# Performance work log

Measured on AMD Instinct MI355X. Metric: run time of the kernel, lower is better.

Reference implementation:

```python
import jax, jax.numpy as jnp
import numpy as np

HIDDEN = 1024
NUM_HEAD = 16
HEAD_DIM = HIDDEN // NUM_HEAD


def setup_inputs() -> dict:
    key = jax.random.key(0)
    ks = jax.random.split(key, 9)
    B, S = 1, 4096
    scale = 1.0 / np.sqrt(HIDDEN)
    inp = {
        "x": jax.random.normal(ks[0], (B, S, HIDDEN), dtype=jnp.float32),
        "wq": jax.random.normal(ks[1], (HIDDEN, HIDDEN), dtype=jnp.float32) * scale,
        "bq": jnp.zeros((HIDDEN,), dtype=jnp.float32),
        "wk": jax.random.normal(ks[2], (HIDDEN, HIDDEN), dtype=jnp.float32) * scale,
        "bk": jnp.zeros((HIDDEN,), dtype=jnp.float32),
        "wv": jax.random.normal(ks[3], (HIDDEN, HIDDEN), dtype=jnp.float32) * scale,
        "bv": jnp.zeros((HIDDEN,), dtype=jnp.float32),
        "wo": jax.random.normal(ks[4], (HIDDEN, HIDDEN), dtype=jnp.float32) * scale,
        "bo": jnp.zeros((HIDDEN,), dtype=jnp.float32),
    }
    return inp


def reference(x, wq, bq, wk, bk, wv, bv, wo, bo):
    B, S, _ = x.shape
    # QKV projections (torch Linear: x @ W.T + b)
    def split_heads(t):
        return t.reshape(B, S, NUM_HEAD, HEAD_DIM).transpose(0, 2, 1, 3)  # [B,H,S,D]
    q = split_heads(x @ wq.T + bq)
    k = split_heads(x @ wk.T + bk)
    v = split_heads(x @ wv.T + bv)
    # scaled dot-product scores: [B,H,S,S]
    scores = jnp.einsum('bhsd,bhtd->bhst', q, k) / jnp.sqrt(jnp.float32(HEAD_DIM))
    # faithful double softmax over the key axis (no mask; dropout = eval identity)
    attn = jax.nn.softmax(scores, axis=-1)
    attn = jax.nn.softmax(attn, axis=-1)
    out = jnp.einsum('bhst,bhtd->bhsd', attn, v)  # [B,H,S,D]
    out = out.transpose(0, 2, 1, 3).reshape(B, S, HIDDEN)
    return out @ wo.T + bo
```

## Files before the change

### kernel.cpp

```cpp
#include <hip/hip_runtime.h>
#include <hip/hip_bf16.h>
#include <stdint.h>

#define S 4096
#define HID 1024
#define NH 16
#define DH 64

typedef __attribute__((ext_vector_type(8))) short short8;
typedef __attribute__((ext_vector_type(2))) float f32x2;
typedef __attribute__((ext_vector_type(4))) float f32x4;
typedef __attribute__((ext_vector_type(16))) float f32x16;
typedef __attribute__((ext_vector_type(4))) unsigned int u32x4;

__device__ __forceinline__ unsigned short f2bf(float f) {
  unsigned int u = __builtin_bit_cast(unsigned int, f);
  u += 0x7FFF + ((u >> 16) & 1);
  return (unsigned short)(u >> 16);
}
__device__ __forceinline__ unsigned int pktrunc(float lo, float hi) {
  return __builtin_amdgcn_perm(__builtin_bit_cast(unsigned int, hi),
                               __builtin_bit_cast(unsigned int, lo), 0x07060302u);
}
__device__ __forceinline__ void gload16(const unsigned short* g, unsigned short* l) {
  __builtin_amdgcn_global_load_lds((const __attribute__((address_space(1))) unsigned int*)g,
                                   (__attribute__((address_space(3))) unsigned int*)l, 16, 0, 0);
}

__global__ __launch_bounds__(256) void cast_kernel(
    const float* __restrict__ x,  const float* __restrict__ wq,
    const float* __restrict__ wk, const float* __restrict__ wv,
    const float* __restrict__ wo,
    unsigned short* __restrict__ xb,  unsigned short* __restrict__ wqb,
    unsigned short* __restrict__ wkb, unsigned short* __restrict__ wvb,
    unsigned short* __restrict__ wob)
{
  int y = blockIdx.y;
  const float* src; unsigned short* dst; int n;
  if      (y == 0) { src = x;  dst = xb;  n = S * HID; }
  else if (y == 1) { src = wq; dst = wqb; n = HID * HID; }
  else if (y == 2) { src = wk; dst = wkb; n = HID * HID; }
  else if (y == 3) { src = wv; dst = wvb; n = HID * HID; }
  else             { src = wo; dst = wob; n = HID * HID; }
  int i = (blockIdx.x * 256 + threadIdx.x) * 4;
  if (i < n) {
    float4 v = *reinterpret_cast<const float4*>(src + i);
    ushort4 o;
    o.x = f2bf(v.x); o.y = f2bf(v.y); o.z = f2bf(v.z); o.w = f2bf(v.w);
    *reinterpret_cast<ushort4*>(dst + i) = o;
  }
}

__device__ __forceinline__ void gemm128(
    const unsigned short* __restrict__ A, const unsigned short* __restrict__ W,
    unsigned short* As, unsigned short* Bs, f32x4 acc[4][4], int row0, int col0)
{
  const int tid = threadIdx.x;
  const int wave = tid >> 6, lane = tid & 63, quad = lane >> 4, l16 = lane & 15;
  const int wr = (wave >> 1) * 64, wc = (wave & 1) * 64;
  const int srow = lane >> 2, sseg = lane & 3;
  const f32x4 z = {0.f, 0.f, 0.f, 0.f};
  #pragma unroll
  for (int i = 0; i < 4; i++)
    #pragma unroll
    for (int j = 0; j < 4; j++) acc[i][j] = z;

  for (int k0 = 0; k0 < HID; k0 += 32) {
    __syncthreads();
    #pragma unroll
    for (int c = 0; c < 2; c++) {
      const int rbase = c * 64 + wave * 16;
      gload16(A + (size_t)(row0 + rbase + srow) * HID + k0 + sseg * 8, As + rbase * 32);
      gload16(W + (size_t)(col0 + rbase + srow) * HID + k0 + sseg * 8, Bs + rbase * 32);
    }
    __syncthreads();

    short8 af[4], bfr[4];
    #pragma unroll
    for (int i = 0; i < 4; i++)
      af[i] = *reinterpret_cast<const short8*>(As + (wr + i * 16 + l16) * 32 + quad * 8);
    #pragma unroll
    for (int j = 0; j < 4; j++)
      bfr[j] = *reinterpret_cast<const short8*>(Bs + (wc + j * 16 + l16) * 32 + quad * 8);
    #pragma unroll
    for (int i = 0; i < 4; i++)
      #pragma unroll
      for (int j = 0; j < 4; j++)
        acc[i][j] = __builtin_amdgcn_mfma_f32_16x16x32_bf16(af[i], bfr[j], acc[i][j], 0, 0, 0);
  }
}

__global__ __launch_bounds__(256) void qkv_gemm_kernel(
    const unsigned short* __restrict__ X,
    const unsigned short* __restrict__ Wq, const unsigned short* __restrict__ Wk,
    const unsigned short* __restrict__ Wv,
    const float* __restrict__ bq, const float* __restrict__ bk, const float* __restrict__ bv,
    unsigned short* __restrict__ Qo, unsigned short* __restrict__ K2o, unsigned short* __restrict__ Vbo)
{
  __shared__ unsigned short As[128 * 32];
  __shared__ unsigned short Bs[128 * 32];
  const int zsel = blockIdx.z;
  const unsigned short* W = (zsel == 0) ? Wq : (zsel == 1) ? Wk : Wv;
  const float* bias        = (zsel == 0) ? bq : (zsel == 1) ? bk : bv;
  const int row0 = blockIdx.x * 128, col0 = blockIdx.y * 128;
  f32x4 acc[4][4];
  gemm128(X, W, As, Bs, acc, row0, col0);

  const int tid = threadIdx.x;
  const int wave = tid >> 6, lane = tid & 63, quad = lane >> 4, l16 = lane & 15;
  const int wr = (wave >> 1) * 64, wc = (wave & 1) * 64;

  if (zsel == 0) {
    const float osc = 0.18033688011112042f;
    #pragma unroll
    for (int j = 0; j < 4; j++) {
      int n = col0 + wc + j * 16 + l16;
      float bb = bias[n];
      int h = n >> 6, d = n & 63;
      #pragma unroll
      for (int i = 0; i < 4; i++)
        #pragma unroll
        for (int rr = 0; rr < 4; rr++) {
          int s = row0 + wr + i * 16 + quad * 4 + rr;
          Qo[(size_t)(h * S + s) * DH + d] = f2bf((acc[i][j][rr] + bb) * osc);
        }
    }
  } else if (zsel == 1) {
    #pragma unroll
    for (int j = 0; j < 4; j++) {
      int n = col0 + wc + j * 16 + l16;
      float bb = bias[n];
      int h = n >> 6, dh = n & 63;
      int c = dh >> 4, hfk = (dh >> 3) & 1, j8 = dh & 7;
      #pragma unroll
      for (int i = 0; i < 4; i++)
        #pragma unroll
        for (int rr = 0; rr < 4; rr++) {
          int s = row0 + wr + i * 16 + quad * 4 + rr;
          int g = s >> 5, l32k = s & 31;
          K2o[((size_t)((h * 128 + g) * 4 + c) * 64 + hfk * 32 + l32k) * 8 + j8] =
              f2bf(acc[i][j][rr] + bb);
        }
    }
  } else {
    #pragma unroll
    for (int j = 0; j < 4; j++) {
      int n = col0 + wc + j * 16 + l16;
      float bb = bias[n];
      int h = n >> 6, dh = n & 63;
      int ng = dh >> 5, l32v = dh & 31;
      int hf_v = quad & 1, jj0 = (quad >> 1) * 4;
      #pragma unroll
      for (int i = 0; i < 4; i++) {
        int gt = (row0 + wr + i * 16) >> 5;
        int grp = i & 1;
        ushort4 pv;
        pv.x = f2bf(acc[i][j][0] + bb); pv.y = f2bf(acc[i][j][1] + bb);
        pv.z = f2bf(acc[i][j][2] + bb); pv.w = f2bf(acc[i][j][3] + bb);
        *reinterpret_cast<ushort4*>(
            Vbo + ((size_t)(((h * 128 + gt) * 2 + grp) * 2 + ng) * 64 + hf_v * 32 + l32v) * 8 + jj0) = pv;
      }
    }
  }
}

__global__ __launch_bounds__(256) void out_gemm_kernel(
    const unsigned short* __restrict__ A, const unsigned short* __restrict__ W,
    const float* __restrict__ be, float* __restrict__ dst)
{
  __shared__ unsigned short As[128 * 32];
  __shared__ unsigned short Bs[128 * 32];
  const int row0 = blockIdx.x * 128, col0 = blockIdx.y * 128;
  f32x4 acc[4][4];
  gemm128(A, W, As, Bs, acc, row0, col0);

  const int tid = threadIdx.x;
  const int wave = tid >> 6, lane = tid & 63, quad = lane >> 4, l16 = lane & 15;
  const int wr = (wave >> 1) * 64, wc = (wave & 1) * 64;
  #pragma unroll
  for (int j = 0; j < 4; j++) {
    int n = col0 + wc + j * 16 + l16;
    float bb = be[n];
    #pragma unroll
    for (int i = 0; i < 4; i++)
      #pragma unroll
      for (int rr = 0; rr < 4; rr++) {
        int s = row0 + wr + i * 16 + quad * 4 + rr;
        dst[(size_t)s * HID + n] = acc[i][j][rr] + bb;
      }
  }
}

__global__ __launch_bounds__(256) void vsum_kernel(
    const unsigned short* __restrict__ Vb, float* __restrict__ VsumP)
{
  __shared__ float red[256];
  const int p = blockIdx.x, h = blockIdx.y, tid = threadIdx.x;
  const int d = tid & 63, chunk = tid >> 6;
  const int ng = d >> 5, l32 = d & 31;
  float s = 0.f;
  for (int m = 0; m < 4; m++) {
    int gt = p * 16 + chunk * 4 + m;
    #pragma unroll
    for (int grp = 0; grp < 2; grp++)
      #pragma unroll
      for (int hf = 0; hf < 2; hf++) {
        uint4 u = *reinterpret_cast<const uint4*>(
            Vb + ((size_t)(((h * 128 + gt) * 2 + grp) * 2 + ng) * 64 + hf * 32 + l32) * 8);
        const unsigned int w[4] = {u.x, u.y, u.z, u.w};
        #pragma unroll
        for (int q = 0; q < 4; q++) {
          s += __builtin_bit_cast(float, w[q] << 16);
          s += __builtin_bit_cast(float, w[q] & 0xFFFF0000u);
        }
      }
  }
  red[tid] = s;
  __syncthreads();
  if (tid < 64)
    VsumP[p * 1024 + h * 64 + tid] = red[tid] + red[64 + tid] + red[128 + tid] + red[192 + tid];
}

__global__ __launch_bounds__(256) void biasfold_kernel(
    const float* __restrict__ VsumP, const float* __restrict__ wo,
    const float* __restrict__ bo, float* __restrict__ be)
{
  const int n = blockIdx.x * 4 + (threadIdx.x >> 6);
  const int l = threadIdx.x & 63;
  float acc = 0.f;
  #pragma unroll
  for (int i = 0; i < 16; i++) {
    float vs = 0.f;
    #pragma unroll
    for (int p = 0; p < 8; p++) vs += VsumP[p * 1024 + l + 64 * i];
    acc += vs * wo[(size_t)n * HID + l + 64 * i];
  }
  #pragma unroll
  for (int off = 32; off >= 1; off >>= 1) acc += __shfl_xor(acc, off);
  if (l == 0) be[n] = bo[n] + acc * (1.f / 4097.f);
}

struct AttnState {
  short8 qf[4];
  f32x16 Oa[2];
  f32x16 zacc;
  f32x2  zp;
};

template<int BUF>
__device__ __forceinline__ void attn_compute(
    const unsigned short* kbase, const unsigned short* vbase, AttnState& st)
{
  short8 kf[4], vfr[4];
  #pragma unroll
  for (int c = 0; c < 4; c++)
    kf[c] = *reinterpret_cast<const short8*>(kbase + BUF * 8192 + c * 512);
  #pragma unroll
  for (int w = 0; w < 4; w++)
    vfr[w] = *reinterpret_cast<const short8*>(vbase + BUF * 8192 + w * 512);

  f32x16 acc = __builtin_amdgcn_mfma_f32_32x32x16_bf16(kf[0], st.qf[0], st.zacc, 0, 0, 0);
  #pragma unroll
  for (int c = 1; c < 4; c++)
    acc = __builtin_amdgcn_mfma_f32_32x32x16_bf16(kf[c], st.qf[c], acc, 0, 0, 0);

  unsigned int D[8];
  #pragma unroll
  for (int m = 0; m < 8; m++) {
    float t0 = __builtin_amdgcn_exp2f(acc[2 * m]);
    float t1 = __builtin_amdgcn_exp2f(acc[2 * m + 1]);
    f32x2 t = {t0, t1};
    st.zp += t;
    D[m] = pktrunc(t0, t1);
  }
  u32x4 d0 = {D[0], D[1], D[2], D[3]};
  u32x4 d1 = {D[4], D[5], D[6], D[7]};
  short8 A0 = __builtin_bit_cast(short8, d0);
  short8 A1 = __builtin_bit_cast(short8, d1);

  st.Oa[0] = __builtin_amdgcn_mfma_f32_32x32x16_bf16(A0, vfr[0], st.Oa[0], 0, 0, 0);
  st.Oa[1] = __builtin_amdgcn_mfma_f32_32x32x16_bf16(A0, vfr[1], st.Oa[1], 0, 0, 0);
  st.Oa[0] = __builtin_amdgcn_mfma_f32_32x32x16_bf16(A1, vfr[2], st.Oa[0], 0, 0, 0);
  st.Oa[1] = __builtin_amdgcn_mfma_f32_32x32x16_bf16(A1, vfr[3], st.Oa[1], 0, 0, 0);
}

__device__ __forceinline__ void stage4(const unsigned short* gs, unsigned short* ldst) {
  #pragma unroll
  for (int i = 0; i < 4; i++)
    gload16(gs + i * 512, ldst + i * 512);
}

__global__ __launch_bounds__(256, 4) void attn_kernel(
    const unsigned short* __restrict__ Q, const unsigned short* __restrict__ K2,
    const unsigned short* __restrict__ Vb, unsigned short* __restrict__ OUT)
{
  __shared__ unsigned short T[2][2][2][2048];
  float* Ol  = reinterpret_cast<float*>(&T[0][0][0][0]);
  float* Z1l = reinterpret_cast<float*>(
      reinterpret_cast<char*>(&T[0][0][0][0]) + 16384);

  const int lin = blockIdx.y * 64 + blockIdx.x;
  const int xcd = lin & 7, idx = lin >> 3;
  const int h = xcd * 2 + (idx >> 6);
  const int q0 = (idx & 63) * 64;

  const int tid = threadIdx.x;
  const int wave = tid >> 6, lane = tid & 63, hf = lane >> 5, l32 = lane & 31;
  const int qc = wave & 1, ks = wave >> 1;

  AttnState st;
  {
    const unsigned short* qrow = Q + (size_t)(h * S + q0 + qc * 32 + l32) * DH;
    #pragma unroll
    for (int c = 0; c < 4; c++)
      st.qf[c] = *reinterpret_cast<const short8*>(qrow + c * 16 + hf * 8);
  }
  #pragma unroll
  for (int r = 0; r < 16; r++) { st.zacc[r] = 0.f; st.Oa[0][r] = 0.f; st.Oa[1][r] = 0.f; }
  st.zp = (f32x2){0.f, 0.f};

  const unsigned short* Kb = K2 + (size_t)h * 128 * 4 * 64 * 8;
  const unsigned short* Vbb = Vb + (size_t)h * 128 * 4 * 64 * 8;

  const int sks = wave >> 1, sv = wave & 1;
  const unsigned short* gs =
      (sv ? Vbb : Kb) + (size_t)sks * 64 * 2048 + (size_t)lane * 8;
  unsigned short* stT0 = &T[0][sks][sv][0];
  unsigned short* stT1 = &T[1][sks][sv][0];

  const unsigned short* kbase = &T[0][ks][0][0] + lane * 8;
  const unsigned short* vbase = &T[0][ks][1][0] + lane * 8;

  stage4(gs, stT0);
  gs += 2048;
  __syncthreads();

  for (int t = 0; t < 31; t++) {
    stage4(gs, stT1); gs += 2048;
    attn_compute<0>(kbase, vbase, st);
    __syncthreads();
    stage4(gs, stT0); gs += 2048;
    attn_compute<1>(kbase, vbase, st);
    __syncthreads();
  }
  stage4(gs, stT1);
  attn_compute<0>(kbase, vbase, st);
  __syncthreads();
  attn_compute<1>(kbase, vbase, st);
  __syncthreads();

  {
    float z1p = st.zp[0] + st.zp[1];
    float z1 = z1p + __shfl_xor(z1p, 32);
    if (hf == 0) Z1l[ks * 64 + qc * 32 + l32] = z1;
  }
  if (ks == 0) {
    #pragma unroll
    for (int reg = 0; reg < 16; reg++) {
      const int row = (reg & 3) + 8 * (reg >> 2) + 4 * hf;
      #pragma unroll
      for (int ng = 0; ng < 2; ng++)
        Ol[(qc * 32 + row) * 64 + ng * 32 + l32] = st.Oa[ng][reg];
    }
  }
  __syncthreads();
  if (ks == 1) {
    #pragma unroll
    for (int reg = 0; reg < 16; reg++) {
      const int row = (reg & 3) + 8 * (reg >> 2) + 4 * hf;
      const int ql = qc * 32 + row;
      const float rz = 1.f / ((Z1l[ql] + Z1l[64 + ql]) * 4097.f);
      const int s = q0 + ql;
      #pragma unroll
      for (int ng = 0; ng < 2; ng++) {
        const float o = Ol[(qc * 32 + row) * 64 + ng * 32 + l32] + st.Oa[ng][reg];
        OUT[(size_t)s * HID + h * DH + ng * 32 + l32] = f2bf(o * rz);
      }
    }
  }
}

extern "C" void kernel_launch(void* const* d_in, const int* in_sizes, int n_in,
                              void* d_out, int out_size, void* d_ws, size_t ws_size,
                              hipStream_t stream) {
  const float* x  = (const float*)d_in[0];
  const float* wq = (const float*)d_in[1];
  const float* bq = (const float*)d_in[2];
  const float* wk = (const float*)d_in[3];
  const float* bk = (const float*)d_in[4];
  const float* wv = (const float*)d_in[5];
  const float* bv = (const float*)d_in[6];
  const float* wo = (const float*)d_in[7];
  const float* bo = (const float*)d_in[8];
  float* out = (float*)d_out;

  char* ws = (char*)d_ws;
  unsigned short* xb  = (unsigned short*)(ws);
  unsigned short* wqb = (unsigned short*)(ws + (8u  << 20));
  unsigned short* wkb = (unsigned short*)(ws + (10u << 20));
  unsigned short* wvb = (unsigned short*)(ws + (12u << 20));
  unsigned short* wob = (unsigned short*)(ws + (14u << 20));
  unsigned short* qw  = (unsigned short*)(ws + (16u << 20));
  unsigned short* k2  = (unsigned short*)(ws + (24u << 20));
  unsigned short* vb  = (unsigned short*)(ws + (32u << 20));
  float* vsump        = (float*)(ws + (40u << 20));
  float* be           = (float*)(ws + (40u << 20) + 65536);
  unsigned short* aw  = xb;

  cast_kernel<<<dim3(4096, 5), 256, 0, stream>>>(x, wq, wk, wv, wo, xb, wqb, wkb, wvb, wob);
  qkv_gemm_kernel<<<dim3(32, 8, 3), 256, 0, stream>>>(xb, wqb, wkb, wvb, bq, bk, bv, qw, k2, vb);
  vsum_kernel<<<dim3(8, 16), 256, 0, stream>>>(vb, vsump);
  biasfold_kernel<<<dim3(256), 256, 0, stream>>>(vsump, wo, bo, be);
  attn_kernel<<<dim3(64, 16), 256, 0, stream>>>(qw, k2, vb, aw);
  out_gemm_kernel<<<dim3(32, 8, 1), 256, 0, stream>>>(aw, wob, be, out);
}
```

Measured before the change: 242.5 us.

## Give each wave private K/V tiles and sync with vmcnt instead of barriers

Restructures the attention kernel so each of the four waves handles all 64 queries against its own quarter of the key sequence. Each wave stages its own K and V tiles into private double-buffered LDS with async global-to-LDS loads and waits on vmcnt instead of block-wide __syncthreads. This is meant to remove per-tile barrier stalls and let each K/V fragment feed two query halves. In exchange it doubles accumulator registers and LDS use (launch bounds drop to 2 blocks per SM) and adds a four-way cross-wave reduction at the end with vectorized bf16 stores.

```diff
diff --git a/kernel.cpp b/kernel.cpp
--- a/kernel.cpp
+++ b/kernel.cpp
@@ -12,6 +12,9 @@
 typedef __attribute__((ext_vector_type(4))) float f32x4;
 typedef __attribute__((ext_vector_type(16))) float f32x16;
 typedef __attribute__((ext_vector_type(4))) unsigned int u32x4;
+
+#define VMCNT8 asm volatile("s_waitcnt vmcnt(8)" ::: "memory")
+#define VMCNT0 asm volatile("s_waitcnt vmcnt(0)" ::: "memory")
 
 __device__ __forceinline__ unsigned short f2bf(float f) {
   unsigned int u = __builtin_bit_cast(unsigned int, f);
@@ -241,10 +244,10 @@
 }
 
 struct AttnState {
-  short8 qf[4];
-  f32x16 Oa[2];
+  short8 qf[2][4];
+  f32x16 Oa[2][2];
   f32x16 zacc;
-  f32x2  zp;
+  f32x2  zp[2];
 };
 
 template<int BUF>
@@ -254,50 +257,56 @@
   short8 kf[4], vfr[4];
   #pragma unroll
   for (int c = 0; c < 4; c++)
-    kf[c] = *reinterpret_cast<const short8*>(kbase + BUF * 8192 + c * 512);
+    kf[c] = *reinterpret_cast<const short8*>(kbase + BUF * 4096 + c * 512);
   #pragma unroll
   for (int w = 0; w < 4; w++)
-    vfr[w] = *reinterpret_cast<const short8*>(vbase + BUF * 8192 + w * 512);
-
-  f32x16 acc = __builtin_amdgcn_mfma_f32_32x32x16_bf16(kf[0], st.qf[0], st.zacc, 0, 0, 0);
-  #pragma unroll
-  for (int c = 1; c < 4; c++)
-    acc = __builtin_amdgcn_mfma_f32_32x32x16_bf16(kf[c], st.qf[c], acc, 0, 0, 0);
-
-  unsigned int D[8];
-  #pragma unroll
-  for (int m = 0; m < 8; m++) {
-    float t0 = __builtin_amdgcn_exp2f(acc[2 * m]);
-    float t1 = __builtin_amdgcn_exp2f(acc[2 * m + 1]);
-    f32x2 t = {t0, t1};
-    st.zp += t;
-    D[m] = pktrunc(t0, t1);
-  }
-  u32x4 d0 = {D[0], D[1], D[2], D[3]};
-  u32x4 d1 = {D[4], D[5], D[6], D[7]};
-  short8 A0 = __builtin_bit_cast(short8, d0);
-  short8 A1 = __builtin_bit_cast(short8, d1);
-
-  st.Oa[0] = __builtin_amdgcn_mfma_f32_32x32x16_bf16(A0, vfr[0], st.Oa[0], 0, 0, 0);
-  st.Oa[1] = __builtin_amdgcn_mfma_f32_32x32x16_bf16(A0, vfr[1], st.Oa[1], 0, 0, 0);
-  st.Oa[0] = __builtin_amdgcn_mfma_f32_32x32x16_bf16(A1, vfr[2], st.Oa[0], 0, 0, 0);
-  st.Oa[1] = __builtin_amdgcn_mfma_f32_32x32x16_bf16(A1, vfr[3], st.Oa[1], 0, 0, 0);
-}
-
-__device__ __forceinline__ void stage4(const unsigned short* gs, unsigned short* ldst) {
-  #pragma unroll
-  for (int i = 0; i < 4; i++)
-    gload16(gs + i * 512, ldst + i * 512);
-}
-
-__global__ __launch_bounds__(256, 4) void attn_kernel(
+    vfr[w] = *reinterpret_cast<const short8*>(vbase + BUF * 4096 + w * 512);
+
+  #pragma unroll
+  for (int qh = 0; qh < 2; qh++) {
+    f32x16 acc = __builtin_amdgcn_mfma_f32_32x32x16_bf16(kf[0], st.qf[qh][0], st.zacc, 0, 0, 0);
+    #pragma unroll
+    for (int c = 1; c < 4; c++)
+      acc = __builtin_amdgcn_mfma_f32_32x32x16_bf16(kf[c], st.qf[qh][c], acc, 0, 0, 0);
+
+    unsigned int D[8];
+    #pragma unroll
+    for (int m = 0; m < 8; m++) {
+      float t0 = __builtin_amdgcn_exp2f(acc[2 * m]);
+      float t1 = __builtin_amdgcn_exp2f(acc[2 * m + 1]);
+      f32x2 t = {t0, t1};
+      st.zp[qh] += t;
+      D[m] = pktrunc(t0, t1);
+    }
+    u32x4 dv0 = {D[0], D[1], D[2], D[3]};
+    u32x4 dv1 = {D[4], D[5], D[6], D[7]};
+    short8 A0 = __builtin_bit_cast(short8, dv0);
+    short8 A1 = __builtin_bit_cast(short8, dv1);
+
+    st.Oa[qh][0] = __builtin_amdgcn_mfma_f32_32x32x16_bf16(A0, vfr[0], st.Oa[qh][0], 0, 0, 0);
+    st.Oa[qh][1] = __builtin_amdgcn_mfma_f32_32x32x16_bf16(A0, vfr[1], st.Oa[qh][1], 0, 0, 0);
+    st.Oa[qh][0] = __builtin_amdgcn_mfma_f32_32x32x16_bf16(A1, vfr[2], st.Oa[qh][0], 0, 0, 0);
+    st.Oa[qh][1] = __builtin_amdgcn_mfma_f32_32x32x16_bf16(A1, vfr[3], st.Oa[qh][1], 0, 0, 0);
+  }
+}
+
+__device__ __forceinline__ void stage_tile(
+    const unsigned short* gK, const unsigned short* gV,
+    unsigned short* lK, unsigned short* lV)
+{
+  #pragma unroll
+  for (int i = 0; i < 4; i++) gload16(gK + i * 512, lK + i * 512);
+  #pragma unroll
+  for (int i = 0; i < 4; i++) gload16(gV + i * 512, lV + i * 512);
+}
+
+__global__ __launch_bounds__(256, 2) void attn_kernel(
     const unsigned short* __restrict__ Q, const unsigned short* __restrict__ K2,
     const unsigned short* __restrict__ Vb, unsigned short* __restrict__ OUT)
 {
-  __shared__ unsigned short T[2][2][2][2048];
-  float* Ol  = reinterpret_cast<float*>(&T[0][0][0][0]);
-  float* Z1l = reinterpret_cast<float*>(
-      reinterpret_cast<char*>(&T[0][0][0][0]) + 16384);
+  __shared__ unsigned short T[4][2][2][2048];
+  __shared__ float Zl[256];
+  float* Ored = reinterpret_cast<float*>(&T[0][0][0][0]);
 
   const int lin = blockIdx.y * 64 + blockIdx.x;
   const int xcd = lin & 7, idx = lin >> 3;
@@ -306,77 +315,106 @@
 
   const int tid = threadIdx.x;
   const int wave = tid >> 6, lane = tid & 63, hf = lane >> 5, l32 = lane & 31;
-  const int qc = wave & 1, ks = wave >> 1;
 
   AttnState st;
+  #pragma unroll
+  for (int qh = 0; qh < 2; qh++) {
+    const unsigned short* qrow = Q + (size_t)(h * S + q0 + qh * 32 + l32) * DH;
+    #pragma unroll
+    for (int c = 0; c < 4; c++)
+      st.qf[qh][c] = *reinterpret_cast<const short8*>(qrow + c * 16 + hf * 8);
+  }
+  #pragma unroll
+  for (int r = 0; r < 16; r++) {
+    st.zacc[r] = 0.f;
+    st.Oa[0][0][r] = 0.f; st.Oa[0][1][r] = 0.f;
+    st.Oa[1][0][r] = 0.f; st.Oa[1][1][r] = 0.f;
+  }
+  st.zp[0] = (f32x2){0.f, 0.f};
+  st.zp[1] = (f32x2){0.f, 0.f};
+
+  const unsigned short* Kb  = K2 + (size_t)h * 128 * 2048;
+  const unsigned short* Vbb = Vb + (size_t)h * 128 * 2048;
+
+  const unsigned short* gK = Kb  + (size_t)wave * 2048 + (size_t)lane * 8;
+  const unsigned short* gV = Vbb + (size_t)wave * 2048 + (size_t)lane * 8;
+  unsigned short* lK0 = &T[wave][0][0][0];
+  unsigned short* lV0 = &T[wave][0][1][0];
+  unsigned short* lK1 = &T[wave][1][0][0];
+  unsigned short* lV1 = &T[wave][1][1][0];
+  const unsigned short* kbase = &T[wave][0][0][0] + lane * 8;
+  const unsigned short* vbase = &T[wave][0][1][0] + lane * 8;
+  const ptrdiff_t STR = 4 * 2048;
+
+  stage_tile(gK, gV, lK0, lV0); gK += STR; gV += STR;
+
+  for (int t = 0; t < 15; t++) {
+    stage_tile(gK, gV, lK1, lV1); gK += STR; gV += STR;
+    VMCNT8;
+    attn_compute<0>(kbase, vbase, st);
+    stage_tile(gK, gV, lK0, lV0); gK += STR; gV += STR;
+    VMCNT8;
+    attn_compute<1>(kbase, vbase, st);
+  }
+  stage_tile(gK, gV, lK1, lV1);
+  VMCNT8;
+  attn_compute<0>(kbase, vbase, st);
+  VMCNT0;
+  attn_compute<1>(kbase, vbase, st);
+
+  __syncthreads();
   {
-    const unsigned short* qrow = Q + (size_t)(h * S + q0 + qc * 32 + l32) * DH;
-    #pragma unroll
-    for (int c = 0; c < 4; c++)
-      st.qf[c] = *reinterpret_cast<const short8*>(qrow + c * 16 + hf * 8);
-  }
-  #pragma unroll
-  for (int r = 0; r < 16; r++) { st.zacc[r] = 0.f; st.Oa[0][r] = 0.f; st.Oa[1][r] = 0.f; }
-  st.zp = (f32x2){0.f, 0.f};
-
-  const unsigned short* Kb = K2 + (size_t)h * 128 * 4 * 64 * 8;
-  const unsigned short* Vbb = Vb + (size_t)h * 128 * 4 * 64 * 8;
-
-  const int sks = wave >> 1, sv = wave & 1;
-  const unsigned short* gs =
-      (sv ? Vbb : Kb) + (size_t)sks * 64 * 2048 + (size_t)lane * 8;
-  unsigned short* stT0 = &T[0][sks][sv][0];
-  unsigned short* stT1 = &T[1][sks][sv][0];
-
-  const unsigned short* kbase = &T[0][ks][0][0] + lane * 8;
-  const unsigned short* vbase = &T[0][ks][1][0] + lane * 8;
-
-  stage4(gs, stT0);
-  gs += 2048;
+    float za = st.zp[0][0] + st.zp[0][1];
+    float zb = st.zp[1][0] + st.zp[1][1];
+    za += __shfl_xor(za, 32);
+    zb += __shfl_xor(zb, 32);
+    if (hf == 0) {
+      Zl[wave * 64 + l32]      = za;
+      Zl[wave * 64 + 32 + l32] = zb;
+    }
+    float* Ow = Ored + wave * 4096;
+    #pragma unroll
+    for (int qh = 0; qh < 2; qh++)
+      #pragma unroll
+      for (int ng = 0; ng < 2; ng++)
+        #pragma unroll
+        for (int r = 0; r < 16; r++) {
+          const int row = (r & 3) + 8 * (r >> 2) + 4 * hf;
+          Ow[(qh * 32 + row) * 64 + ng * 32 + l32] = st.Oa[qh][ng][r];
+        }
+  }
   __syncthreads();
-
-  for (int t = 0; t < 31; t++) {
-    stage4(gs, stT1); gs += 2048;
-    attn_compute<0>(kbase, vbase, st);
-    __syncthreads();
-    stage4(gs, stT0); gs += 2048;
-    attn_compute<1>(kbase, vbase, st);
-    __syncthreads();
-  }
-  stage4(gs, stT1);
-  attn_compute<0>(kbase, vbase, st);
-  __syncthreads();
-  attn_compute<1>(kbase, vbase, st);
-  __syncthreads();
-
   {
-    float z1p = st.zp[0] + st.zp[1];
-    float z1 = z1p + __shfl_xor(z1p, 32);
-    if (hf == 0) Z1l[ks * 64 + qc * 32 + l32] = z1;
-  }
-  if (ks == 0) {
-    #pragma unroll
-    for (int reg = 0; reg < 16; reg++) {
-      const int row = (reg & 3) + 8 * (reg >> 2) + 4 * hf;
-      #pragma unroll
-      for (int ng = 0; ng < 2; ng++)
-        Ol[(qc * 32 + row) * 64 + ng * 32 + l32] = st.Oa[ng][reg];
-    }
-  }
-  __syncthreads();
-  if (ks == 1) {
-    #pragma unroll
-    for (int reg = 0; reg < 16; reg++) {
-      const int row = (reg & 3) + 8 * (reg >> 2) + 4 * hf;
-      const int ql = qc * 32 + row;
-      const float rz = 1.f / ((Z1l[ql] + Z1l[64 + ql]) * 4097.f);
-      const int s = q0 + ql;
-      #pragma unroll
-      for (int ng = 0; ng < 2; ng++) {
-        const float o = Ol[(qc * 32 + row) * 64 + ng * 32 + l32] + st.Oa[ng][reg];
-        OUT[(size_t)s * HID + h * DH + ng * 32 + l32] = f2bf(o * rz);
-      }
-    }
+    const int q = tid >> 2, d0 = (tid & 3) * 16;
+    const float* O0 = Ored + q * 64 + d0;
+    f32x4 s0 = *reinterpret_cast<const f32x4*>(O0);
+    f32x4 s1 = *reinterpret_cast<const f32x4*>(O0 + 4);
+    f32x4 s2 = *reinterpret_cast<const f32x4*>(O0 + 8);
+    f32x4 s3 = *reinterpret_cast<const f32x4*>(O0 + 12);
+    #pragma unroll
+    for (int w = 1; w < 4; w++) {
+      const float* Ow = Ored + w * 4096 + q * 64 + d0;
+      s0 += *reinterpret_cast<const f32x4*>(Ow);
+      s1 += *reinterpret_cast<const f32x4*>(Ow + 4);
+      s2 += *reinterpret_cast<const f32x4*>(Ow + 8);
+      s3 += *reinterpret_cast<const f32x4*>(Ow + 12);
+    }
+    const float zt = Zl[q] + Zl[64 + q] + Zl[128 + q] + Zl[192 + q];
+    const float rz = 1.f / (zt * 4097.f);
+    unsigned short* op = OUT + (size_t)(q0 + q) * HID + h * DH + d0;
+    ushort4 u;
+    u.x = f2bf(s0[0] * rz); u.y = f2bf(s0[1] * rz);
+    u.z = f2bf(s0[2] * rz); u.w = f2bf(s0[3] * rz);
+    *reinterpret_cast<ushort4*>(op) = u;
+    u.x = f2bf(s1[0] * rz); u.y = f2bf(s1[1] * rz);
+    u.z = f2bf(s1[2] * rz); u.w = f2bf(s1[3] * rz);
+    *reinterpret_cast<ushort4*>(op + 4) = u;
+    u.x = f2bf(s2[0] * rz); u.y = f2bf(s2[1] * rz);
+    u.z = f2bf(s2[2] * rz); u.w = f2bf(s2[3] * rz);
+    *reinterpret_cast<ushort4*>(op + 8) = u;
+    u.x = f2bf(s3[0] * rz); u.y = f2bf(s3[1] * rz);
+    u.z = f2bf(s3[2] * rz); u.w = f2bf(s3[3] * rz);
+    *reinterpret_cast<ushort4*>(op + 12) = u;
   }
 }
 
```

Measured after the change: 238.9 us. Within noise of the previous version (-1.5%).
